# Performance work log

Measured on AMD Instinct MI355X. Metric: run time of the kernel, lower is better.

## Reference

```python
import jax, jax.numpy as jnp
import numpy as np

N = 100_000      # nodes
E = 1_600_000    # edges
F_IN = 64        # num_features
H = 64           # hidden_dim
G = 128          # graphs in batch
BN_EPS = 1e-5


def _gcn_conv(x, W, b, row, col, ew, n_nodes):
    """PyG GCNConv with edge weights, self-loops, symmetric normalization."""
    # add self loops (weight 1.0)
    loops = jnp.arange(n_nodes, dtype=row.dtype)
    r = jnp.concatenate([row, loops])
    c = jnp.concatenate([col, loops])
    w = jnp.concatenate([ew, jnp.ones((n_nodes,), ew.dtype)])
    # deg over destination (col), as in PyG gcn_norm
    deg = jax.ops.segment_sum(w, c, num_segments=n_nodes)
    dinv = jnp.where(deg > 0, jax.lax.rsqrt(deg), 0.0)
    norm = dinv[r] * w * dinv[c]          # [E+N]
    h = x @ W                             # [N, H] small GEMM
    msg = h[r] * norm[:, None]            # gather + scale, [E+N, H]
    out = jax.ops.segment_sum(msg, c, num_segments=n_nodes)  # scatter-add
    return out + b


def _bn_eval(x, gamma, beta, mean, var):
    return (x - mean) * jax.lax.rsqrt(var + BN_EPS) * gamma + beta


def setup_inputs() -> dict:
    key = jax.random.key(0)
    ks = jax.random.split(key, 10)
    x = jax.random.normal(ks[0], (N, F_IN), jnp.float32)
    edge_index = jax.random.randint(ks[1], (2, E), 0, N, dtype=jnp.int32)
    edge_weight = jax.random.uniform(ks[2], (E,), jnp.float32)
    batch = jnp.sort(jax.random.randint(ks[3], (N,), 0, G, dtype=jnp.int32))

    def lin(k, i, o):
        return jax.random.normal(k, (i, o), jnp.float32) / np.float32(np.sqrt(i))

    d = {
        "x": x, "edge_index": edge_index, "edge_weight": edge_weight, "batch": batch,
        "W1": lin(ks[4], F_IN, H), "b1": jnp.zeros((H,), jnp.float32),
        "W2": lin(ks[5], H, H),    "b2": jnp.zeros((H,), jnp.float32),
        "W3": lin(ks[6], H, H),    "b3": jnp.zeros((H,), jnp.float32),
        "Wfc": lin(ks[7], H, 1),   "bfc": jnp.zeros((1,), jnp.float32),
    }
    for i in (1, 2, 3):
        d[f"g{i}"] = jnp.ones((H,), jnp.float32)   # BN gamma
        d[f"be{i}"] = jnp.zeros((H,), jnp.float32)  # BN beta
        d[f"m{i}"] = jnp.zeros((H,), jnp.float32)   # BN running mean
        d[f"v{i}"] = jnp.ones((H,), jnp.float32)    # BN running var
    return d


def reference(x, edge_index, edge_weight, batch,
              W1, b1, W2, b2, W3, b3, Wfc, bfc,
              g1, be1, m1, v1, g2, be2, m2, v2, g3, be3, m3, v3):
    row, col = edge_index[0], edge_index[1]
    h = _gcn_conv(x, W1, b1, row, col, edge_weight, N)
    h = _bn_eval(jax.nn.relu(h), g1, be1, m1, v1)
    h = _gcn_conv(h, W2, b2, row, col, edge_weight, N)
    h = _bn_eval(jax.nn.relu(h), g2, be2, m2, v2)
    h = _gcn_conv(h, W3, b3, row, col, edge_weight, N)
    h = _bn_eval(h, g3, be3, m3, v3)               # note: no ReLU before bn3
    pooled = jax.ops.segment_sum(h, batch, num_segments=G)  # global_add_pool
    pooled = jax.nn.relu(pooled)                   # dropout is identity in eval
    return (pooled @ Wfc + bfc).reshape(-1)        # [G]
```

## Files before the change

### kernel.cpp

```cpp
#include <hip/hip_runtime.h>
#include <hip/hip_fp16.h>

#define BN_EPS 1e-5f
#define FIXP 1048576.0f
#define FIXP_INV (1.0f / 1048576.0f)
#define EPB 4096
#define PADCAP 4608
#define FP8_SCALE 16.0f
#define FP8_INV (1.0f / 16.0f)
#define W15_INV (1.0f / 32768.0f)

typedef __attribute__((ext_vector_type(2))) float vfloat2;
typedef __attribute__((ext_vector_type(8))) short short8;
typedef __attribute__((ext_vector_type(4))) float f32x4;

__device__ __forceinline__ float fatomic_add(float* p, float v) {
    return unsafeAtomicAdd(p, v);
}

__device__ __forceinline__ unsigned short f2bf(float f) {
    unsigned int u = __float_as_uint(f);
    return (unsigned short)((u + 0x7FFFu + ((u >> 16) & 1u)) >> 16);
}

__global__ __launch_bounds__(256) void k_binscatter(const int* __restrict__ rowi,
                                                    const int* __restrict__ coli,
                                                    const float* __restrict__ ew,
                                                    unsigned int* __restrict__ binCursor,
                                                    int2* __restrict__ staged,
                                                    float* __restrict__ pooled,
                                                    int E, int NB, int G64) {
    __shared__ unsigned int h[512];
    __shared__ unsigned int bb[512];
    int tid = threadIdx.x;
    if (blockIdx.x == 0)
        for (int i = tid; i < G64; i += 256) pooled[i] = 0.f;
    for (int i = tid; i < 512; i += 256) h[i] = 0;
    __syncthreads();
    int base = blockIdx.x * EPB;
    int lim = min(EPB, E - base);
    unsigned short rank[16];
    int nj = (lim - tid + 255) / 256;
    for (int j = 0; j < nj; ++j) {
        int e = base + tid + j * 256;
        rank[j] = (unsigned short)atomicAdd(&h[(unsigned)coli[e] >> 8], 1u);
    }
    __syncthreads();
    for (int b = tid; b < NB; b += 256)
        bb[b] = h[b] ? atomicAdd(&binCursor[b], h[b]) : 0u;
    __syncthreads();
    for (int j = 0; j < nj; ++j) {
        int e = base + tid + j * 256;
        unsigned int c = (unsigned)coli[e];
        unsigned int b = c >> 8;
        int2 rec;
        rec.x = rowi[e] | (int)((c & 255u) << 24);
        rec.y = __float_as_int(ew[e]);
        staged[(size_t)b * PADCAP + bb[b] + rank[j]] = rec;
    }
}

__global__ __launch_bounds__(256) void k_binfinal(const int2* __restrict__ staged,
                                                  const unsigned int* __restrict__ binCursor,
                                                  unsigned int* __restrict__ csr,
                                                  int2* __restrict__ se,
                                                  float* __restrict__ dinv,
                                                  int N) {
    __shared__ int2 recs[PADCAP];
    __shared__ unsigned int cnt[256];
    __shared__ unsigned int deg[256];
    __shared__ int sc[256];
    __shared__ unsigned int cur[256];
    int tid = threadIdx.x;
    int b = blockIdx.x;
    int s0 = b * PADCAP;
    int n = (int)binCursor[b];
    cnt[tid] = 0;
    deg[tid] = 0;
    __syncthreads();
    for (int i = tid; i < n; i += 256) {
        int2 rec = staged[s0 + i];
        recs[i] = rec;
        unsigned int cl = ((unsigned)rec.x >> 24) & 255u;
        atomicAdd(&cnt[cl], 1u);
        float w = __int_as_float(rec.y);
        atomicAdd(&deg[cl], (unsigned int)(w * FIXP));
    }
    __syncthreads();
    int v = (int)cnt[tid];
    sc[tid] = v;
    __syncthreads();
    for (int off = 1; off < 256; off <<= 1) {
        int add = (tid >= off) ? sc[tid - off] : 0;
        __syncthreads();
        sc[tid] += add;
        __syncthreads();
    }
    int lpre = sc[tid] - v;
    cur[tid] = (unsigned int)lpre;
    int c = b * 256 + tid;
    if (c < N) {
        se[c] = make_int2(s0 + lpre, s0 + lpre + v);
        dinv[c] = rsqrtf(1.0f + (float)deg[tid] * FIXP_INV);
    }
    __syncthreads();
    for (int i = tid; i < n; i += 256) {
        int2 rec = recs[i];
        unsigned int cl = ((unsigned)rec.x >> 24) & 255u;
        unsigned int p = atomicAdd(&cur[cl], 1u);
        float w = __int_as_float(rec.y);
        unsigned int wq = min((unsigned int)(w * 32768.f + 0.5f), 32767u);
        csr[s0 + p] = (wq << 17) | ((unsigned)rec.x & 0x1FFFFu);
    }
}

__global__ __launch_bounds__(256) void k_gemm(const float* __restrict__ x,
                                              const float* __restrict__ W,
                                              const float* __restrict__ dinv,
                                              int* __restrict__ th4, int n) {
    __shared__ short Wt[64][72];
    __shared__ short xs[16][72];
    __shared__ float outs[16][68];
    int tid = threadIdx.x;
    for (int i = tid; i < 4096; i += 256) {
        int k = i >> 6, nn = i & 63;
        Wt[nn][k] = (short)f2bf(W[i]);
    }
    int row0 = blockIdx.x * 16;
    int nrows = min(16, n - row0);
    {
        int r = tid >> 4, c4 = (tid & 15) * 4;
        float4 v = make_float4(0.f, 0.f, 0.f, 0.f);
        if (r < nrows)
            v = ((const float4*)(x + (size_t)(row0 + r) * 64))[tid & 15];
        xs[r][c4 + 0] = (short)f2bf(v.x);
        xs[r][c4 + 1] = (short)f2bf(v.y);
        xs[r][c4 + 2] = (short)f2bf(v.z);
        xs[r][c4 + 3] = (short)f2bf(v.w);
    }
    __syncthreads();
    int wv = tid >> 6, lane = tid & 63;
    int mn = lane & 15, kg = (lane >> 4) * 8;
    f32x4 acc = {0.f, 0.f, 0.f, 0.f};
    short8 a0 = *(const short8*)&xs[mn][kg];
    short8 a1 = *(const short8*)&xs[mn][kg + 32];
    short8 b0 = *(const short8*)&Wt[wv * 16 + mn][kg];
    short8 b1 = *(const short8*)&Wt[wv * 16 + mn][kg + 32];
    acc = __builtin_amdgcn_mfma_f32_16x16x32_bf16(a0, b0, acc, 0, 0, 0);
    acc = __builtin_amdgcn_mfma_f32_16x16x32_bf16(a1, b1, acc, 0, 0, 0);
#pragma unroll
    for (int r = 0; r < 4; ++r)
        outs[(lane >> 4) * 4 + r][wv * 16 + mn] = acc[r];
    __syncthreads();
    int rl = tid >> 4, fq = tid & 15;
    if (rl < nrows) {
        float d = dinv[row0 + rl] * FP8_SCALE;
        float4 o = *(const float4*)&outs[rl][fq * 4];
        int p = __builtin_amdgcn_cvt_pk_fp8_f32(o.x * d, o.y * d, 0, false);
        p = __builtin_amdgcn_cvt_pk_fp8_f32(o.z * d, o.w * d, p, true);
        th4[(row0 + rl) * 16 + fq] = p;
    }
}

__global__ __launch_bounds__(256) void k_fusedgg(const unsigned int* __restrict__ csr,
                                                 const int2* __restrict__ se,
                                                 const int* __restrict__ th4_in,
                                                 const float* __restrict__ dinv,
                                                 const float* __restrict__ bias,
                                                 const float* __restrict__ gam,
                                                 const float* __restrict__ bet,
                                                 const float* __restrict__ mu,
                                                 const float* __restrict__ var,
                                                 const float* __restrict__ Wnext,
                                                 int* __restrict__ th4_out, int n) {
    __shared__ short Wt[64][72];
    __shared__ short xs[16][72];
    __shared__ float outs[16][68];
    int tid = threadIdx.x;
    for (int i = tid; i < 4096; i += 256) {
        int k = i >> 6, nn = i & 63;
        Wt[nn][k] = (short)f2bf(Wnext[i]);
    }
    int w = tid >> 6;
    int lane = tid & 63;
    int q = lane >> 4;
    int l = lane & 15;
    int node = blockIdx.x * 16 + w * 4 + q;
    bool valid = node < n;
    float4 b4 = ((const float4*)bias)[l];
    float4 m4 = ((const float4*)mu)[l];
    float4 v4 = ((const float4*)var)[l];
    float4 G4 = ((const float4*)gam)[l];
    float4 B4 = ((const float4*)bet)[l];
    float4 scf, shf;
    scf.x = rsqrtf(v4.x + BN_EPS) * G4.x;  shf.x = B4.x - m4.x * scf.x;
    scf.y = rsqrtf(v4.y + BN_EPS) * G4.y;  shf.y = B4.y - m4.y * scf.y;
    scf.z = rsqrtf(v4.z + BN_EPS) * G4.z;  shf.z = B4.z - m4.z * scf.z;
    scf.w = rsqrtf(v4.w + BN_EPS) * G4.w;  shf.w = B4.w - m4.w * scf.w;

    float4 av[4];
    av[0] = make_float4(0.f, 0.f, 0.f, 0.f);
    av[1] = av[0]; av[2] = av[0]; av[3] = av[0];
    float4 sf = av[0];
    int e = 0, eend = 0, esafe = 0;
    float dv = 0.f;
    if (valid) {
        int2 ext = se[node];
        e = ext.x; eend = ext.y;
        esafe = (eend > e) ? (eend - 1) : 0;
        dv = dinv[node];
        int sv = th4_in[node * 16 + l];
        vfloat2 lo = __builtin_amdgcn_cvt_pk_f32_fp8(sv, false);
        vfloat2 hi = __builtin_amdgcn_cvt_pk_f32_fp8(sv, true);
        sf = make_float4(lo.x, lo.y, hi.x, hi.y);
    }
    while (__any(e < eend)) {
        if (e < eend) {
            unsigned int cc[8];
            int rr[8];
#pragma unroll
            for (int j = 0; j < 8; ++j)
                cc[j] = __builtin_nontemporal_load(&csr[min(e + j, esafe)]);
#pragma unroll
            for (int j = 0; j < 8; ++j)
                rr[j] = th4_in[(int)((cc[j] & 0x1FFFFu) << 4) + l];
#pragma unroll
            for (int j = 0; j < 8; ++j) {
                float wj = (e + j < eend) ? (float)(cc[j] >> 17) : 0.f;
                vfloat2 lo = __builtin_amdgcn_cvt_pk_f32_fp8(rr[j], false);
                vfloat2 hi = __builtin_amdgcn_cvt_pk_f32_fp8(rr[j], true);
                av[j & 3].x = fmaf(wj, lo.x, av[j & 3].x);
                av[j & 3].y = fmaf(wj, lo.y, av[j & 3].y);
                av[j & 3].z = fmaf(wj, hi.x, av[j & 3].z);
                av[j & 3].w = fmaf(wj, hi.y, av[j & 3].w);
            }
        }
        e += 8;
    }
    float4 res = make_float4(0.f, 0.f, 0.f, 0.f);
    if (valid) {
        float4 acc;
        acc.x = ((av[0].x + av[1].x) + (av[2].x + av[3].x)) * W15_INV + sf.x;
        acc.y = ((av[0].y + av[1].y) + (av[2].y + av[3].y)) * W15_INV + sf.y;
        acc.z = ((av[0].z + av[1].z) + (av[2].z + av[3].z)) * W15_INV + sf.z;
        acc.w = ((av[0].w + av[1].w) + (av[2].w + av[3].w)) * W15_INV + sf.w;
        float d = dv * FP8_INV;
        float r0 = fmaxf(d * acc.x + b4.x, 0.f);
        float r1 = fmaxf(d * acc.y + b4.y, 0.f);
        float r2 = fmaxf(d * acc.z + b4.z, 0.f);
        float r3 = fmaxf(d * acc.w + b4.w, 0.f);
        res.x = r0 * scf.x + shf.x;
        res.y = r1 * scf.y + shf.y;
        res.z = r2 * scf.z + shf.z;
        res.w = r3 * scf.w + shf.w;
    }
    {
        int nl = w * 4 + q;
        union { unsigned short s[4]; int2 i2; } u;
        u.s[0] = f2bf(res.x); u.s[1] = f2bf(res.y);
        u.s[2] = f2bf(res.z); u.s[3] = f2bf(res.w);
        *(int2*)&xs[nl][4 * l] = u.i2;
    }
    __syncthreads();
    int mn = lane & 15, kg = (lane >> 4) * 8;
    f32x4 acc = {0.f, 0.f, 0.f, 0.f};
    short8 a0 = *(const short8*)&xs[mn][kg];
    short8 a1 = *(const short8*)&xs[mn][kg + 32];
    short8 b0 = *(const short8*)&Wt[w * 16 + mn][kg];
    short8 b1 = *(const short8*)&Wt[w * 16 + mn][kg + 32];
    acc = __builtin_amdgcn_mfma_f32_16x16x32_bf16(a0, b0, acc, 0, 0, 0);
    acc = __builtin_amdgcn_mfma_f32_16x16x32_bf16(a1, b1, acc, 0, 0, 0);
#pragma unroll
    for (int r = 0; r < 4; ++r)
        outs[(lane >> 4) * 4 + r][w * 16 + mn] = acc[r];
    __syncthreads();
    int rl = tid >> 4, fq = tid & 15;
    int row = blockIdx.x * 16 + rl;
    if (row < n) {
        float d = dinv[row] * FP8_SCALE;
        float4 o = *(const float4*)&outs[rl][fq * 4];
        int p = __builtin_amdgcn_cvt_pk_fp8_f32(o.x * d, o.y * d, 0, false);
        p = __builtin_amdgcn_cvt_pk_fp8_f32(o.z * d, o.w * d, p, true);
        th4_out[row * 16 + fq] = p;
    }
}

__global__ __launch_bounds__(256) void k_gather(const unsigned int* __restrict__ csr,
                                                const int2* __restrict__ se,
                                                const int* __restrict__ th4,
                                                const float* __restrict__ dinv,
                                                const float* __restrict__ bias,
                                                const float* __restrict__ gam,
                                                const float* __restrict__ bet,
                                                const float* __restrict__ mu,
                                                const float* __restrict__ var,
                                                const int* __restrict__ batch,
                                                float* __restrict__ pooled,
                                                int n) {
    int w = threadIdx.x >> 6;
    int lane = threadIdx.x & 63;
    int q = lane >> 4;
    int l = lane & 15;
    int node = blockIdx.x * 16 + w * 4 + q;
    bool valid = node < n;
    float4 b4 = ((const float4*)bias)[l];
    float4 m4 = ((const float4*)mu)[l];
    float4 v4 = ((const float4*)var)[l];
    float4 G4 = ((const float4*)gam)[l];
    float4 B4 = ((const float4*)bet)[l];
    float4 scf, shf;
    scf.x = rsqrtf(v4.x + BN_EPS) * G4.x;  shf.x = B4.x - m4.x * scf.x;
    scf.y = rsqrtf(v4.y + BN_EPS) * G4.y;  shf.y = B4.y - m4.y * scf.y;
    scf.z = rsqrtf(v4.z + BN_EPS) * G4.z;  shf.z = B4.z - m4.z * scf.z;
    scf.w = rsqrtf(v4.w + BN_EPS) * G4.w;  shf.w = B4.w - m4.w * scf.w;

    float4 av[4];
    av[0] = make_float4(0.f, 0.f, 0.f, 0.f);
    av[1] = av[0]; av[2] = av[0]; av[3] = av[0];
    float4 sf = av[0];
    int e = 0, eend = 0, esafe = 0;
    float dv = 0.f;
    if (valid) {
        int2 ext = se[node];
        e = ext.x; eend = ext.y;
        esafe = (eend > e) ? (eend - 1) : 0;
        dv = dinv[node];
        int sv = th4[node * 16 + l];
        vfloat2 lo = __builtin_amdgcn_cvt_pk_f32_fp8(sv, false);
        vfloat2 hi = __builtin_amdgcn_cvt_pk_f32_fp8(sv, true);
        sf = make_float4(lo.x, lo.y, hi.x, hi.y);
    }
    while (__any(e < eend)) {
        if (e < eend) {
            unsigned int cc[8];
            int rr[8];
#pragma unroll
            for (int j = 0; j < 8; ++j)
                cc[j] = __builtin_nontemporal_load(&csr[min(e + j, esafe)]);
#pragma unroll
            for (int j = 0; j < 8; ++j)
                rr[j] = th4[(int)((cc[j] & 0x1FFFFu) << 4) + l];
#pragma unroll
            for (int j = 0; j < 8; ++j) {
                float wj = (e + j < eend) ? (float)(cc[j] >> 17) : 0.f;
                vfloat2 lo = __builtin_amdgcn_cvt_pk_f32_fp8(rr[j], false);
                vfloat2 hi = __builtin_amdgcn_cvt_pk_f32_fp8(rr[j], true);
                av[j & 3].x = fmaf(wj, lo.x, av[j & 3].x);
                av[j & 3].y = fmaf(wj, lo.y, av[j & 3].y);
                av[j & 3].z = fmaf(wj, hi.x, av[j & 3].z);
                av[j & 3].w = fmaf(wj, hi.y, av[j & 3].w);
            }
        }
        e += 8;
    }
    float4 res = make_float4(0.f, 0.f, 0.f, 0.f);
    if (valid) {
        float4 acc;
        acc.x = ((av[0].x + av[1].x) + (av[2].x + av[3].x)) * W15_INV + sf.x;
        acc.y = ((av[0].y + av[1].y) + (av[2].y + av[3].y)) * W15_INV + sf.y;
        acc.z = ((av[0].z + av[1].z) + (av[2].z + av[3].z)) * W15_INV + sf.z;
        acc.w = ((av[0].w + av[1].w) + (av[2].w + av[3].w)) * W15_INV + sf.w;
        float d = dv * FP8_INV;
        float r0 = d * acc.x + b4.x;
        float r1 = d * acc.y + b4.y;
        float r2 = d * acc.z + b4.z;
        float r3 = d * acc.w + b4.w;
        res.x = r0 * scf.x + shf.x;
        res.y = r1 * scf.y + shf.y;
        res.z = r2 * scf.z + shf.z;
        res.w = r3 * scf.w + shf.w;
    }
    int bid = valid ? batch[node] : -1;
    int bid0 = __shfl(bid, 0);
    bool same = __all(bid == bid0);
    if (same) {
        if (bid0 >= 0) {
            res.x += __shfl_xor(res.x, 16);
            res.y += __shfl_xor(res.y, 16);
            res.z += __shfl_xor(res.z, 16);
            res.w += __shfl_xor(res.w, 16);
            res.x += __shfl_xor(res.x, 32);
            res.y += __shfl_xor(res.y, 32);
            res.z += __shfl_xor(res.z, 32);
            res.w += __shfl_xor(res.w, 32);
            if (q == 0) {
                float* pp = &pooled[bid0 * 64 + 4 * l];
                fatomic_add(pp + 0, res.x);
                fatomic_add(pp + 1, res.y);
                fatomic_add(pp + 2, res.z);
                fatomic_add(pp + 3, res.w);
            }
        }
    } else if (valid) {
        float* pp = &pooled[bid * 64 + 4 * l];
        fatomic_add(pp + 0, res.x);
        fatomic_add(pp + 1, res.y);
        fatomic_add(pp + 2, res.z);
        fatomic_add(pp + 3, res.w);
    }
}

__global__ __launch_bounds__(128) void k_fc(const float* __restrict__ pooled,
                                            const float* __restrict__ Wfc,
                                            const float* __restrict__ bfc,
                                            float* __restrict__ out, int G) {
    int g = threadIdx.x;
    if (g >= G) return;
    float s = bfc[0];
#pragma unroll
    for (int f = 0; f < 64; ++f) s += fmaxf(pooled[g * 64 + f], 0.f) * Wfc[f];
    out[g] = s;
}

extern "C" void kernel_launch(void* const* d_in, const int* in_sizes, int n_in,
                              void* d_out, int out_size, void* d_ws, size_t ws_size,
                              hipStream_t stream) {
    const float* x    = (const float*)d_in[0];
    const int*   eidx = (const int*)d_in[1];
    const float* ew   = (const float*)d_in[2];
    const int*   batch= (const int*)d_in[3];
    const float* W1 = (const float*)d_in[4];
    const float* b1 = (const float*)d_in[5];
    const float* W2 = (const float*)d_in[6];
    const float* b2 = (const float*)d_in[7];
    const float* W3 = (const float*)d_in[8];
    const float* b3 = (const float*)d_in[9];
    const float* Wfc = (const float*)d_in[10];
    const float* bfc = (const float*)d_in[11];
    const float* g1 = (const float*)d_in[12];
    const float* be1 = (const float*)d_in[13];
    const float* m1 = (const float*)d_in[14];
    const float* v1 = (const float*)d_in[15];
    const float* g2 = (const float*)d_in[16];
    const float* be2 = (const float*)d_in[17];
    const float* m2 = (const float*)d_in[18];
    const float* v2 = (const float*)d_in[19];
    const float* g3 = (const float*)d_in[20];
    const float* be3 = (const float*)d_in[21];
    const float* m3 = (const float*)d_in[22];
    const float* v3 = (const float*)d_in[23];

    const int N = in_sizes[0] / 64;
    const int E = in_sizes[1] / 2;
    const int G = out_size;
    const int* rowi = eidx;
    const int* coli = eidx + E;
    const int NB = (N + 255) >> 8;

    char* ws = (char*)d_ws;
    size_t off = 0;
    auto alloc = [&](size_t bytes) {
        char* p = ws + off;
        off += (bytes + 255) & ~(size_t)255;
        return p;
    };
    unsigned int* binCursor = (unsigned int*)alloc(512 * 4);
    float* dinv   = (float*)alloc((size_t)N * 4);
    int2*  se     = (int2*) alloc((size_t)N * 8);
    unsigned int* csr = (unsigned int*)alloc((size_t)NB * PADCAP * 4);
    int*   th4a   = (int*)  alloc((size_t)N * 64);
    int*   th4b   = (int*)  alloc((size_t)N * 64);
    float* pooled = (float*)alloc((size_t)G * 64 * 4);
    int2*  staged = (int2*)alloc((size_t)NB * PADCAP * 8);

    const int bblk = (E + EPB - 1) / EPB;
    const int gblk = (N + 15) / 16;
    const int mblk = (N + 15) / 16;

    hipMemsetAsync(binCursor, 0, 512 * 4, stream);
    k_binscatter<<<bblk, 256, 0, stream>>>(rowi, coli, ew, binCursor, staged,
                                           pooled, E, NB, G * 64);
    k_binfinal<<<NB, 256, 0, stream>>>(staged, binCursor, csr, se, dinv, N);

    k_gemm<<<mblk, 256, 0, stream>>>(x, W1, dinv, th4a, N);
    k_fusedgg<<<gblk, 256, 0, stream>>>(csr, se, th4a, dinv, b1, g1, be1, m1, v1,
                                        W2, th4b, N);
    k_fusedgg<<<gblk, 256, 0, stream>>>(csr, se, th4b, dinv, b2, g2, be2, m2, v2,
                                        W3, th4a, N);
    k_gather<<<gblk, 256, 0, stream>>>(csr, se, th4a, dinv, b3, g3, be3, m3, v3,
                                       batch, pooled, N);
    k_fc<<<1, 128, 0, stream>>>(pooled, Wfc, bfc, (float*)d_out, G);
}
```

Baseline: 359.3 us.

## Quantize staged edge weights early and spread pooling atomics over replicas

Edge weights are quantized to 15-bit integers during bin scatter and stored in a separate ushort array, so the staging buffer shrinks from 8 to 6 bytes per edge. The degree sum is now computed from these quantized weights. The final gather kernel first combines per-wave pooled sums in shared memory, then issues atomics into one of 8 replicated pooled buffers chosen by block index, which k_fc sums at the end. This cuts atomic contention on the 128x64 pool, at the cost of an extra block barrier, slightly coarser degree precision, and a larger reduction in k_fc.

```diff
diff --git a/kernel.cpp b/kernel.cpp
--- a/kernel.cpp
+++ b/kernel.cpp
@@ -2,13 +2,12 @@
 #include <hip/hip_fp16.h>
 
 #define BN_EPS 1e-5f
-#define FIXP 1048576.0f
-#define FIXP_INV (1.0f / 1048576.0f)
 #define EPB 4096
 #define PADCAP 4608
 #define FP8_SCALE 16.0f
 #define FP8_INV (1.0f / 16.0f)
 #define W15_INV (1.0f / 32768.0f)
+#define NPOOL 8
 
 typedef __attribute__((ext_vector_type(2))) float vfloat2;
 typedef __attribute__((ext_vector_type(8))) short short8;
@@ -27,14 +26,15 @@
                                                     const int* __restrict__ coli,
                                                     const float* __restrict__ ew,
                                                     unsigned int* __restrict__ binCursor,
-                                                    int2* __restrict__ staged,
-                                                    float* __restrict__ pooled,
-                                                    int E, int NB, int G64) {
+                                                    int* __restrict__ staged1,
+                                                    unsigned short* __restrict__ staged2,
+                                                    float* __restrict__ pooled8,
+                                                    int E, int NB, int PZ) {
     __shared__ unsigned int h[512];
     __shared__ unsigned int bb[512];
     int tid = threadIdx.x;
     if (blockIdx.x == 0)
-        for (int i = tid; i < G64; i += 256) pooled[i] = 0.f;
+        for (int i = tid; i < PZ; i += 256) pooled8[i] = 0.f;
     for (int i = tid; i < 512; i += 256) h[i] = 0;
     __syncthreads();
     int base = blockIdx.x * EPB;
@@ -53,20 +53,21 @@
         int e = base + tid + j * 256;
         unsigned int c = (unsigned)coli[e];
         unsigned int b = c >> 8;
-        int2 rec;
-        rec.x = rowi[e] | (int)((c & 255u) << 24);
-        rec.y = __float_as_int(ew[e]);
-        staged[(size_t)b * PADCAP + bb[b] + rank[j]] = rec;
-    }
-}
-
-__global__ __launch_bounds__(256) void k_binfinal(const int2* __restrict__ staged,
+        size_t idx = (size_t)b * PADCAP + bb[b] + rank[j];
+        staged1[idx] = rowi[e] | (int)((c & 255u) << 24);
+        staged2[idx] = (unsigned short)min((unsigned int)(ew[e] * 32768.f + 0.5f), 32767u);
+    }
+}
+
+__global__ __launch_bounds__(256) void k_binfinal(const int* __restrict__ staged1,
+                                                  const unsigned short* __restrict__ staged2,
                                                   const unsigned int* __restrict__ binCursor,
                                                   unsigned int* __restrict__ csr,
                                                   int2* __restrict__ se,
                                                   float* __restrict__ dinv,
                                                   int N) {
-    __shared__ int2 recs[PADCAP];
+    __shared__ int recs1[PADCAP];
+    __shared__ unsigned short recs2[PADCAP];
     __shared__ unsigned int cnt[256];
     __shared__ unsigned int deg[256];
     __shared__ int sc[256];
@@ -79,12 +80,13 @@
     deg[tid] = 0;
     __syncthreads();
     for (int i = tid; i < n; i += 256) {
-        int2 rec = staged[s0 + i];
-        recs[i] = rec;
-        unsigned int cl = ((unsigned)rec.x >> 24) & 255u;
+        int r1 = staged1[s0 + i];
+        unsigned short wq = staged2[s0 + i];
+        recs1[i] = r1;
+        recs2[i] = wq;
+        unsigned int cl = (unsigned)r1 >> 24;
         atomicAdd(&cnt[cl], 1u);
-        float w = __int_as_float(rec.y);
-        atomicAdd(&deg[cl], (unsigned int)(w * FIXP));
+        atomicAdd(&deg[cl], (unsigned int)wq);
     }
     __syncthreads();
     int v = (int)cnt[tid];
@@ -101,16 +103,14 @@
     int c = b * 256 + tid;
     if (c < N) {
         se[c] = make_int2(s0 + lpre, s0 + lpre + v);
-        dinv[c] = rsqrtf(1.0f + (float)deg[tid] * FIXP_INV);
+        dinv[c] = rsqrtf(1.0f + (float)deg[tid] * W15_INV);
     }
     __syncthreads();
     for (int i = tid; i < n; i += 256) {
-        int2 rec = recs[i];
-        unsigned int cl = ((unsigned)rec.x >> 24) & 255u;
+        int r1 = recs1[i];
+        unsigned int cl = (unsigned)r1 >> 24;
         unsigned int p = atomicAdd(&cur[cl], 1u);
-        float w = __int_as_float(rec.y);
-        unsigned int wq = min((unsigned int)(w * 32768.f + 0.5f), 32767u);
-        csr[s0 + p] = (wq << 17) | ((unsigned)rec.x & 0x1FFFFu);
+        csr[s0 + p] = ((unsigned int)recs2[i] << 17) | ((unsigned)r1 & 0x1FFFFu);
     }
 }
 
@@ -295,14 +295,17 @@
                                                 const float* __restrict__ mu,
                                                 const float* __restrict__ var,
                                                 const int* __restrict__ batch,
-                                                float* __restrict__ pooled,
-                                                int n) {
+                                                float* __restrict__ pooled8,
+                                                int n, int G64) {
+    __shared__ float vals[4][64];
+    __shared__ int wbid[4];
     int w = threadIdx.x >> 6;
     int lane = threadIdx.x & 63;
     int q = lane >> 4;
     int l = lane & 15;
     int node = blockIdx.x * 16 + w * 4 + q;
     bool valid = node < n;
+    float* myPool = pooled8 + (size_t)(blockIdx.x & (NPOOL - 1)) * G64;
     float4 b4 = ((const float4*)bias)[l];
     float4 m4 = ((const float4*)mu)[l];
     float4 v4 = ((const float4*)var)[l];
@@ -374,41 +377,62 @@
     int bid0 = __shfl(bid, 0);
     bool same = __all(bid == bid0);
     if (same) {
-        if (bid0 >= 0) {
-            res.x += __shfl_xor(res.x, 16);
-            res.y += __shfl_xor(res.y, 16);
-            res.z += __shfl_xor(res.z, 16);
-            res.w += __shfl_xor(res.w, 16);
-            res.x += __shfl_xor(res.x, 32);
-            res.y += __shfl_xor(res.y, 32);
-            res.z += __shfl_xor(res.z, 32);
-            res.w += __shfl_xor(res.w, 32);
-            if (q == 0) {
-                float* pp = &pooled[bid0 * 64 + 4 * l];
-                fatomic_add(pp + 0, res.x);
-                fatomic_add(pp + 1, res.y);
-                fatomic_add(pp + 2, res.z);
-                fatomic_add(pp + 3, res.w);
+        res.x += __shfl_xor(res.x, 16);
+        res.y += __shfl_xor(res.y, 16);
+        res.z += __shfl_xor(res.z, 16);
+        res.w += __shfl_xor(res.w, 16);
+        res.x += __shfl_xor(res.x, 32);
+        res.y += __shfl_xor(res.y, 32);
+        res.z += __shfl_xor(res.z, 32);
+        res.w += __shfl_xor(res.w, 32);
+        if (q == 0) ((float4*)&vals[w][0])[l] = res;
+        if (lane == 0) wbid[w] = bid0;
+    } else {
+        if (valid) {
+            float* pp = myPool + bid * 64 + 4 * l;
+            fatomic_add(pp + 0, res.x);
+            fatomic_add(pp + 1, res.y);
+            fatomic_add(pp + 2, res.z);
+            fatomic_add(pp + 3, res.w);
+        }
+        if (lane == 0) wbid[w] = -1;
+    }
+    __syncthreads();
+    if (w == 0) {
+        int f = threadIdx.x;
+        float s2 = 0.f;
+        int cur = -1;
+#pragma unroll
+        for (int i = 0; i < 4; ++i) {
+            int bi = wbid[i];
+            if (bi < 0) continue;
+            if (bi == cur) {
+                s2 += vals[i][f];
+            } else {
+                if (cur >= 0) fatomic_add(&myPool[cur * 64 + f], s2);
+                cur = bi;
+                s2 = vals[i][f];
             }
         }
-    } else if (valid) {
-        float* pp = &pooled[bid * 64 + 4 * l];
-        fatomic_add(pp + 0, res.x);
-        fatomic_add(pp + 1, res.y);
-        fatomic_add(pp + 2, res.z);
-        fatomic_add(pp + 3, res.w);
-    }
-}
-
-__global__ __launch_bounds__(128) void k_fc(const float* __restrict__ pooled,
+        if (cur >= 0) fatomic_add(&myPool[cur * 64 + f], s2);
+    }
+}
+
+__global__ __launch_bounds__(128) void k_fc(const float* __restrict__ pooled8,
                                             const float* __restrict__ Wfc,
                                             const float* __restrict__ bfc,
                                             float* __restrict__ out, int G) {
     int g = threadIdx.x;
     if (g >= G) return;
+    int G64 = G * 64;
     float s = bfc[0];
-#pragma unroll
-    for (int f = 0; f < 64; ++f) s += fmaxf(pooled[g * 64 + f], 0.f) * Wfc[f];
+#pragma unroll 4
+    for (int f = 0; f < 64; ++f) {
+        float p = 0.f;
+#pragma unroll
+        for (int c = 0; c < NPOOL; ++c) p += pooled8[c * G64 + g * 64 + f];
+        s += fmaxf(p, 0.f) * Wfc[f];
+    }
     out[g] = s;
 }
 
@@ -460,17 +484,20 @@
     unsigned int* csr = (unsigned int*)alloc((size_t)NB * PADCAP * 4);
     int*   th4a   = (int*)  alloc((size_t)N * 64);
     int*   th4b   = (int*)  alloc((size_t)N * 64);
-    float* pooled = (float*)alloc((size_t)G * 64 * 4);
-    int2*  staged = (int2*)alloc((size_t)NB * PADCAP * 8);
+    float* pooled8 = (float*)alloc((size_t)NPOOL * G * 64 * 4);
+    int*   staged1 = (int*)alloc((size_t)NB * PADCAP * 4);
+    unsigned short* staged2 = (unsigned short*)alloc((size_t)NB * PADCAP * 2);
 
     const int bblk = (E + EPB - 1) / EPB;
     const int gblk = (N + 15) / 16;
     const int mblk = (N + 15) / 16;
 
     hipMemsetAsync(binCursor, 0, 512 * 4, stream);
-    k_binscatter<<<bblk, 256, 0, stream>>>(rowi, coli, ew, binCursor, staged,
-                                           pooled, E, NB, G * 64);
-    k_binfinal<<<NB, 256, 0, stream>>>(staged, binCursor, csr, se, dinv, N);
+    k_binscatter<<<bblk, 256, 0, stream>>>(rowi, coli, ew, binCursor, staged1,
+                                           staged2, pooled8, E, NB,
+                                           NPOOL * G * 64);
+    k_binfinal<<<NB, 256, 0, stream>>>(staged1, staged2, binCursor, csr, se,
+                                       dinv, N);
 
     k_gemm<<<mblk, 256, 0, stream>>>(x, W1, dinv, th4a, N);
     k_fusedgg<<<gblk, 256, 0, stream>>>(csr, se, th4a, dinv, b1, g1, be1, m1, v1,
@@ -478,6 +505,6 @@
     k_fusedgg<<<gblk, 256, 0, stream>>>(csr, se, th4b, dinv, b2, g2, be2, m2, v2,
                                         W3, th4a, N);
     k_gather<<<gblk, 256, 0, stream>>>(csr, se, th4a, dinv, b3, g3, be3, m3, v3,
-                                       batch, pooled, N);
-    k_fc<<<1, 128, 0, stream>>>(pooled, Wfc, bfc, (float*)d_out, G);
-}
+                                       batch, pooled8, N, G * 64);
+    k_fc<<<1, 128, 0, stream>>>(pooled8, Wfc, bfc, (float*)d_out, G);
+}
```

Measured after the change: 322.5 us. -10.2%, faster.
